# Kernel optimization log

Measured on AMD Instinct MI355X. Metric: run time of the kernel, lower is better.

## Reference

```python
import jax, jax.numpy as jnp
import numpy as np

B, C_IN, L = 8, 12, 4096
D = 64        # mamba_in_ch
DI = 2 * D    # d_inner (expand=2)
DS = 16       # d_state
DC = 4        # d_conv
DTR = 4       # dt_rank = ceil(D/16)
R = 10        # pixel-shuffle / upsample factor
K = 15        # big conv kernel size

def _p(key, shape, scale=0.05):
    return (jax.random.normal(key, shape) * scale).astype(jnp.float32)

def setup_inputs() -> dict:
    key = jax.random.key(0)
    ks = jax.random.split(key, 12)
    return dict(
        x=jax.random.normal(ks[0], (B, C_IN, L), jnp.float32),
        conv_in_w=_p(ks[1], (D, C_IN, K)), conv_in_b=jnp.zeros((D,), jnp.float32),
        in_proj_w=_p(ks[2], (2 * DI, D)),
        dw_conv_w=_p(ks[3], (DI, 1, DC)), dw_conv_b=jnp.zeros((DI,), jnp.float32),
        x_proj_w=_p(ks[4], (DTR + 2 * DS, DI)),
        dt_proj_w=_p(ks[5], (DI, DTR)), dt_proj_b=_p(ks[6], (DI,)),
        A_log=jnp.log(jnp.tile(jnp.arange(1, DS + 1, dtype=jnp.float32)[None, :], (DI, 1))),
        D_ssm=jnp.ones((DI,), jnp.float32),
        out_proj_w=_p(ks[7], (D, DI)),
        conv_merge_w=_p(ks[8], (D, D, K)), conv_merge_b=jnp.zeros((D,), jnp.float32),
        bn_gamma=jnp.ones((D,), jnp.float32), bn_beta=jnp.zeros((D,), jnp.float32),
        conv_ps1_w=_p(ks[9], (R * C_IN, D, K)), conv_ps1_b=jnp.zeros((R * C_IN,), jnp.float32),
    )

def conv1d(x, w, b, pad_l, pad_r, groups=1):
    out = jax.lax.conv_general_dilated(x, w, (1,), [(pad_l, pad_r)],
        dimension_numbers=('NCH', 'OIH', 'NCH'), feature_group_count=groups)
    return out + b[None, :, None]

def mamba_layer(x, in_proj_w, dw_w, dw_b, x_proj_w, dt_proj_w, dt_proj_b, A_log, D_ssm, out_proj_w):
    # x: (B, L, D)
    xz = jnp.einsum('bld,ed->ble', x, in_proj_w)          # (B,L,2*DI)
    xs, z = jnp.split(xz, 2, axis=-1)
    xc = jnp.transpose(xs, (0, 2, 1))                      # (B,DI,L)
    xc = conv1d(xc, dw_w, dw_b, DC - 1, 0, groups=DI)      # causal depthwise conv, truncated to L
    xs = jax.nn.silu(jnp.transpose(xc, (0, 2, 1)))         # (B,L,DI)
    dbl = jnp.einsum('bld,ed->ble', xs, x_proj_w)          # (B,L,DTR+2*DS)
    dt, Bm, Cm = jnp.split(dbl, [DTR, DTR + DS], axis=-1)
    dt = jax.nn.softplus(jnp.einsum('blr,dr->bld', dt, dt_proj_w) + dt_proj_b)  # (B,L,DI)
    A = -jnp.exp(A_log)                                    # (DI,DS)
    dA = jnp.exp(dt[..., None] * A)                        # (B,L,DI,DS)
    dBx = dt[..., None] * Bm[:, :, None, :] * xs[..., None]

    def step(h, inputs):
        dA_t, dBx_t, C_t = inputs                          # (B,DI,DS),(B,DI,DS),(B,DS)
        h = dA_t * h + dBx_t
        y = jnp.einsum('bds,bs->bd', h, C_t)
        return h, y

    h0 = jnp.zeros((x.shape[0], DI, DS), x.dtype)
    _, ys = jax.lax.scan(step, h0,
        (jnp.transpose(dA, (1, 0, 2, 3)), jnp.transpose(dBx, (1, 0, 2, 3)), jnp.transpose(Cm, (1, 0, 2))))
    y = jnp.transpose(ys, (1, 0, 2)) + xs * D_ssm          # (B,L,DI)
    y = y * jax.nn.silu(z)
    return jnp.einsum('bld,ed->ble', y, out_proj_w)        # (B,L,D)

def reference(x, conv_in_w, conv_in_b, in_proj_w, dw_conv_w, dw_conv_b, x_proj_w,
              dt_proj_w, dt_proj_b, A_log, D_ssm, out_proj_w,
              conv_merge_w, conv_merge_b, bn_gamma, bn_beta, conv_ps1_w, conv_ps1_b):
    pad = (K - 1) // 2
    x_in = jax.nn.leaky_relu(conv1d(x, conv_in_w, conv_in_b, pad, pad), 0.01)  # (B,64,L)
    xm = jnp.transpose(x_in, (0, 2, 1))
    xm = xm + mamba_layer(xm, in_proj_w, dw_conv_w, dw_conv_b, x_proj_w,
                          dt_proj_w, dt_proj_b, A_log, D_ssm, out_proj_w)     # n_layer=1, residual
    xm = jnp.transpose(xm, (0, 2, 1))                                          # (B,64,L)
    xmerge = conv1d(xm, conv_merge_w, conv_merge_b, pad, pad)
    mean = jnp.mean(xmerge, axis=(0, 2), keepdims=True)                        # BatchNorm1d (training stats)
    var = jnp.var(xmerge, axis=(0, 2), keepdims=True)
    xmerge = (xmerge - mean) * jax.lax.rsqrt(var + 1e-5) * bn_gamma[None, :, None] + bn_beta[None, :, None]
    xmerge = xmerge + x_in
    xp = conv1d(xmerge, conv_ps1_w, conv_ps1_b, pad, pad)                      # (B,120,L)
    # PixelShuffle1D(r=10): (B, r*Cout, L) -> (B, Cout, L*r)
    Bn, ch, Ln = xp.shape
    ps = xp.reshape(Bn, R, ch // R, Ln).transpose(0, 2, 3, 1).reshape(Bn, ch // R, Ln * R)
    # F.interpolate(x, scale_factor=10, mode='linear', align_corners=False)
    out_len = L * R
    src = jnp.maximum((jnp.arange(out_len, dtype=jnp.float32) + 0.5) / R - 0.5, 0.0)
    i0 = jnp.minimum(jnp.floor(src).astype(jnp.int32), L - 1)
    i1 = jnp.minimum(i0 + 1, L - 1)
    frac = src - i0.astype(jnp.float32)
    up = x[..., i0] * (1.0 - frac) + x[..., i1] * frac
    return ps + up
```

## Files before the change

kernel.cpp:

```cpp
#include <hip/hip_runtime.h>
#include <math.h>

#define BB 8
#define CIN 12
#define LL 4096
#define DD 64
#define DIx 128
#define DSx 16
#define RR 10
#define KK 15
#define NCH 256
#define CLEN 16
#define OUTL 40960

typedef __attribute__((ext_vector_type(8))) short s8v;
typedef __attribute__((ext_vector_type(8))) __bf16 b8v;
typedef __attribute__((ext_vector_type(4))) float f4v;
union frag_u { s8v s; b8v b; };

__device__ __forceinline__ unsigned short f2b(float f) {
    unsigned int u = __float_as_uint(f);
    u = (u + 0x7fffu + ((u >> 16) & 1u)) >> 16;
    return (unsigned short)u;
}
__device__ __forceinline__ float b2f(unsigned short h) {
    return __uint_as_float(((unsigned int)h) << 16);
}

template<int CI, int CO, int COT, bool LEAKY>
__global__ __launch_bounds__(256) void k_conv(const float* __restrict__ in,
        const float* __restrict__ w, const float* __restrict__ bias,
        float* __restrict__ out) {
    const int LT = 1024;
    int tid = threadIdx.x;
    int bid = blockIdx.x;
    const int nlt = LL / LT;
    const int ncog = CO / COT;
    int lt = bid % nlt;
    int cog = (bid / nlt) % ncog;
    int b = bid / (nlt * ncog);
    int l0 = lt * LT + tid * 4;
    int co0 = cog * COT;

    float acc[COT][4];
#pragma unroll
    for (int c = 0; c < COT; ++c) {
        float bv = bias[co0 + c];
#pragma unroll
        for (int j = 0; j < 4; ++j) acc[c][j] = bv;
    }
    for (int ci = 0; ci < CI; ++ci) {
        const float* inp = in + ((size_t)b * CI + ci) * LL;
        float in20[20];
#pragma unroll
        for (int q = 0; q < 5; ++q) {
            int gi = l0 - 8 + q * 4;
            if (gi >= 0 && gi + 3 < LL) {
                float4 v = *(const float4*)(inp + gi);
                in20[q*4+0] = v.x; in20[q*4+1] = v.y;
                in20[q*4+2] = v.z; in20[q*4+3] = v.w;
            } else {
#pragma unroll
                for (int j = 0; j < 4; ++j) {
                    int g = gi + j;
                    in20[q*4+j] = (g >= 0 && g < LL) ? inp[g] : 0.f;
                }
            }
        }
#pragma unroll
        for (int c = 0; c < COT; ++c) {
            const float* wp = w + ((size_t)(co0 + c) * CI + ci) * KK;
#pragma unroll
            for (int k = 0; k < KK; ++k) {
                float wv = wp[k];
#pragma unroll
                for (int j = 0; j < 4; ++j)
                    acc[c][j] += wv * in20[j + k + 1];
            }
        }
    }
#pragma unroll
    for (int c = 0; c < COT; ++c) {
        float r[4];
#pragma unroll
        for (int j = 0; j < 4; ++j) {
            float v = acc[c][j];
            if (LEAKY) v = (v >= 0.f) ? v : 0.01f * v;
            r[j] = v;
        }
        *(float4*)(out + ((size_t)b * CO + co0 + c) * LL + l0) =
            make_float4(r[0], r[1], r[2], r[3]);
    }
}

template<int CO_REAL, int NCOB>
__global__ __launch_bounds__(256) void k_wprep(const float* __restrict__ w,
        unsigned short* __restrict__ wp) {
    int idx = blockIdx.x * 256 + threadIdx.x;
    if (idx >= 15 * NCOB * 1024) return;
    int j = idx & 7;
    int lane = (idx >> 3) & 63;
    int cis = (idx >> 9) & 1;
    int rest = idx >> 10;
    int cob = rest % NCOB;
    int kk = rest / NCOB;
    int co = cob * 16 + (lane & 15);
    int ci = cis * 32 + ((lane >> 4) << 3) + j;
    float val = (co < CO_REAL) ? w[((size_t)co * 64 + ci) * KK + kk] : 0.f;
    wp[idx] = f2b(val);
}

template<int CO_REAL, int NCOB, int MODE>
__global__ __launch_bounds__(256) void k_convmfma(
        const unsigned short* __restrict__ xt,
        const unsigned short* __restrict__ wp,
        const float* __restrict__ bias, void* __restrict__ outv) {
    __shared__ unsigned short in_lds[142 * 72];
    const int NCOT = NCOB / 4;
    int tid = threadIdx.x;
    int bid = blockIdx.x;
    int lt = bid & 31;
    int cot = (bid >> 5) % NCOT;
    int b = bid / (32 * NCOT);
    int l0 = lt * 128;
#pragma unroll
    for (int i = 0; i < 5; ++i) {
        int q = i * 256 + tid;
        if (q < 1136) {
            int r = q >> 3, c8 = (q & 7) * 8;
            int gl = l0 - 7 + r;
            s8v v = {0,0,0,0,0,0,0,0};
            if (gl >= 0 && gl < LL)
                v = *(const s8v*)&xt[((size_t)b * LL + gl) * 64 + c8];
            *(s8v*)&in_lds[r * 72 + c8] = v;
        }
    }
    __syncthreads();
    int lane = tid & 63, wv = tid >> 6;
    int corow = (lane >> 4) << 2;
    f4v acc[4][2];
#pragma unroll
    for (int mt = 0; mt < 4; ++mt) {
#pragma unroll
        for (int r = 0; r < 4; ++r) {
            int co = cot * 64 + mt * 16 + corow + r;
            float bv = (co < CO_REAL) ? bias[co] : 0.f;
            acc[mt][0][r] = bv;
            acc[mt][1][r] = bv;
        }
    }
    int bcol = lane & 15;
    int cig = (lane >> 4) << 3;
    for (int k = 0; k < KK; ++k) {
#pragma unroll
        for (int cis = 0; cis < 2; ++cis) {
            frag_u a[4], bf[2];
#pragma unroll
            for (int mt = 0; mt < 4; ++mt)
                a[mt].s = *(const s8v*)&wp[((((k * NCOB + cot * 4 + mt) * 2 + cis) << 9)
                                           + (lane << 3))];
#pragma unroll
            for (int nt = 0; nt < 2; ++nt)
                bf[nt].s = *(const s8v*)&in_lds[(wv * 32 + nt * 16 + bcol + k) * 72
                                               + cis * 32 + cig];
#pragma unroll
            for (int mt = 0; mt < 4; ++mt)
#pragma unroll
                for (int nt = 0; nt < 2; ++nt)
                    acc[mt][nt] = __builtin_amdgcn_mfma_f32_16x16x32_bf16(
                        a[mt].b, bf[nt].b, acc[mt][nt], 0, 0, 0);
        }
    }
#pragma unroll
    for (int mt = 0; mt < 4; ++mt)
#pragma unroll
        for (int nt = 0; nt < 2; ++nt) {
            int l = l0 + wv * 32 + nt * 16 + bcol;
#pragma unroll
            for (int r = 0; r < 4; ++r) {
                int co = cot * 64 + mt * 16 + corow + r;
                if (co < CO_REAL) {
                    if (MODE == 0)
                        ((float*)outv)[((size_t)b * CO_REAL + co) * LL + l] = acc[mt][nt][r];
                    else
                        ((unsigned short*)outv)[((size_t)b * CO_REAL + co) * LL + l]
                            = f2b(acc[mt][nt][r]);
                }
            }
        }
}

__global__ __launch_bounds__(256) void k_bnpart(const float* __restrict__ xm,
        float* __restrict__ stats) {
    int c = blockIdx.x >> 3, b = blockIdx.x & 7;
    const float* p = xm + ((size_t)b * DD + c) * LL;
    int tid = threadIdx.x;
    float s = 0.f, ss = 0.f;
#pragma unroll
    for (int it = 0; it < 4; ++it) {
        float4 v = *(const float4*)(p + (size_t)(it * 256 + tid) * 4);
        s  += v.x + v.y + v.z + v.w;
        ss += v.x*v.x + v.y*v.y + v.z*v.z + v.w*v.w;
    }
    for (int o = 32; o > 0; o >>= 1) {
        s  += __shfl_down(s, o);
        ss += __shfl_down(ss, o);
    }
    __shared__ float red[8];
    int wid = tid >> 6;
    if ((tid & 63) == 0) { red[wid] = s; red[4 + wid] = ss; }
    __syncthreads();
    if (tid == 0) {
        atomicAdd(&stats[c], red[0] + red[1] + red[2] + red[3]);
        atomicAdd(&stats[64 + c], red[4] + red[5] + red[6] + red[7]);
    }
}

__global__ __launch_bounds__(256) void k_gemm_inproj(const float* __restrict__ A,
        const float* __restrict__ W, unsigned short* __restrict__ C) {
    __shared__ float At[64 * 132];
    __shared__ float Wt[64 * 132];
    int tid = threadIdx.x;
    int bid = blockIdx.x;
    int nb = bid & 1;
    int mb = bid >> 1;
    int row0 = mb * 128;
    int n0 = nb * 128;
    int b = row0 >> 12;
    int l0 = row0 & 4095;
#pragma unroll
    for (int it = 0; it < 8; ++it) {
        int idx = it * 256 + tid;
        int k = idx >> 5, m4 = (idx & 31) * 4;
        float4 v = *(const float4*)(A + ((size_t)b * DD + k) * LL + l0 + m4);
        *(float4*)&At[k * 132 + m4] = v;
    }
#pragma unroll
    for (int it = 0; it < 8; ++it) {
        int lin = it * 1024 + tid * 4;
        int n = lin >> 6, k = lin & 63;
        float4 v = *(const float4*)(W + (size_t)(n0 + n) * 64 + k);
        Wt[(k+0)*132 + n] = v.x; Wt[(k+1)*132 + n] = v.y;
        Wt[(k+2)*132 + n] = v.z; Wt[(k+3)*132 + n] = v.w;
    }
    __syncthreads();
    int tx = tid & 15, ty = tid >> 4;
    float acc[2][2][4][4] = {};
#pragma unroll 4
    for (int k = 0; k < 64; ++k) {
        float4 aLo = *(float4*)&At[k*132 + ty*4];
        float4 aHi = *(float4*)&At[k*132 + 64 + ty*4];
        float4 bLo = *(float4*)&Wt[k*132 + tx*4];
        float4 bHi = *(float4*)&Wt[k*132 + 64 + tx*4];
        float a0[4] = {aLo.x, aLo.y, aLo.z, aLo.w};
        float a1[4] = {aHi.x, aHi.y, aHi.z, aHi.w};
        float b0[4] = {bLo.x, bLo.y, bLo.z, bLo.w};
        float b1[4] = {bHi.x, bHi.y, bHi.z, bHi.w};
#pragma unroll
        for (int mm = 0; mm < 4; ++mm)
#pragma unroll
            for (int nn = 0; nn < 4; ++nn) {
                acc[0][0][mm][nn] += a0[mm] * b0[nn];
                acc[0][1][mm][nn] += a0[mm] * b1[nn];
                acc[1][0][mm][nn] += a1[mm] * b0[nn];
                acc[1][1][mm][nn] += a1[mm] * b1[nn];
            }
    }
#pragma unroll
    for (int qm = 0; qm < 2; ++qm)
#pragma unroll
        for (int mm = 0; mm < 4; ++mm) {
            int row = row0 + qm*64 + ty*4 + mm;
#pragma unroll
            for (int qn = 0; qn < 2; ++qn) {
                unsigned short o[4];
#pragma unroll
                for (int nn = 0; nn < 4; ++nn) o[nn] = f2b(acc[qm][qn][mm][nn]);
                *(uint2*)&C[(size_t)row * 256 + n0 + qn*64 + tx*4] = *(uint2*)o;
            }
        }
}

template<int NW>
__global__ __launch_bounds__(256) void k_gemm64dw(
        const unsigned short* __restrict__ xzb,
        const float* __restrict__ dww, const float* __restrict__ dwb,
        const float* __restrict__ W, float* __restrict__ out) {
    __shared__ float At[64 * 132];
    __shared__ float Wt[64 * 68];
    __shared__ float sdw[128][4];
    __shared__ float sbias[128];
    int tid = threadIdx.x;
    int row0 = blockIdx.x * 128;
    int l0 = row0 & 4095;
    if (tid < 128) {
        *(float4*)&sdw[tid][0] = *(const float4*)(dww + tid * 4);
        sbias[tid] = dwb[tid];
    }
    int tx = tid & 15, ty = tid >> 4;
    float acc[2][4][4] = {};
#pragma unroll
    for (int kt = 0; kt < 2; ++kt) {
        __syncthreads();
#pragma unroll
        for (int it = 0; it < 4; ++it) {
            int task = it * 256 + tid;
            int m = task >> 3;
            int k8 = (task & 7) * 8;
            int d0 = kt * 64 + k8;
            float s[8];
#pragma unroll
            for (int j = 0; j < 8; ++j) s[j] = sbias[d0 + j];
#pragma unroll
            for (int tap = 0; tap < 4; ++tap) {
                if (l0 + m - 3 + tap >= 0) {
                    s8v xv = *(const s8v*)&xzb[(size_t)(row0 + m - 3 + tap) * 256 + d0];
#pragma unroll
                    for (int j = 0; j < 8; ++j)
                        s[j] += b2f((unsigned short)xv[j]) * sdw[d0 + j][tap];
                }
            }
#pragma unroll
            for (int j = 0; j < 8; ++j) {
                float v = s[j];
                At[(k8 + j) * 132 + m] = v / (1.f + __expf(-v));
            }
        }
#pragma unroll
        for (int it = 0; it < 4; ++it) {
            int lin = it * 1024 + tid * 4;
            int n = lin >> 6, k = lin & 63;
            float4 v = make_float4(0.f, 0.f, 0.f, 0.f);
            if (n < NW)
                v = *(const float4*)(W + (size_t)n * 128 + kt*64 + k);
            Wt[(k+0)*68 + n] = v.x; Wt[(k+1)*68 + n] = v.y;
            Wt[(k+2)*68 + n] = v.z; Wt[(k+3)*68 + n] = v.w;
        }
        __syncthreads();
#pragma unroll 4
        for (int k = 0; k < 64; ++k) {
            float4 aLo = *(float4*)&At[k*132 + ty*4];
            float4 aHi = *(float4*)&At[k*132 + 64 + ty*4];
            float4 b4  = *(float4*)&Wt[k*68 + tx*4];
            float a0[4] = {aLo.x, aLo.y, aLo.z, aLo.w};
            float a1[4] = {aHi.x, aHi.y, aHi.z, aHi.w};
            float bv[4] = {b4.x, b4.y, b4.z, b4.w};
#pragma unroll
            for (int mm = 0; mm < 4; ++mm)
#pragma unroll
                for (int nn = 0; nn < 4; ++nn) {
                    acc[0][mm][nn] += a0[mm] * bv[nn];
                    acc[1][mm][nn] += a1[mm] * bv[nn];
                }
        }
    }
#pragma unroll
    for (int qm = 0; qm < 2; ++qm)
#pragma unroll
        for (int mm = 0; mm < 4; ++mm) {
            int row = row0 + qm*64 + ty*4 + mm;
            *(float4*)(out + (size_t)row * 64 + tx*4) =
                make_float4(acc[qm][mm][0], acc[qm][mm][1],
                            acc[qm][mm][2], acc[qm][mm][3]);
        }
}

__global__ __launch_bounds__(256) void k_gemm64_tr(
        const unsigned short* __restrict__ A, const float* __restrict__ W,
        const float* __restrict__ res, unsigned short* __restrict__ out) {
    __shared__ float smem[13312];
    float* At = smem;
    float* Wt = smem + 64*132;
    int tid = threadIdx.x;
    int row0 = blockIdx.x * 128;
    int tx = tid & 15, ty = tid >> 4;
    int b = row0 >> 12, l0 = row0 & 4095;
    float acc[2][4][4] = {};
#pragma unroll
    for (int kt = 0; kt < 2; ++kt) {
        __syncthreads();
#pragma unroll
        for (int it = 0; it < 4; ++it) {
            int task = it * 256 + tid;
            int m = task >> 3;
            int k8 = (task & 7) * 8;
            s8v v = *(const s8v*)&A[(size_t)(row0 + m) * 128 + kt*64 + k8];
#pragma unroll
            for (int j = 0; j < 8; ++j)
                At[(k8 + j) * 132 + m] = b2f((unsigned short)v[j]);
        }
#pragma unroll
        for (int it = 0; it < 4; ++it) {
            int lin = it * 1024 + tid * 4;
            int n = lin >> 6, k = lin & 63;
            float4 v = *(const float4*)(W + (size_t)n * 128 + kt*64 + k);
            Wt[(k+0)*68 + n] = v.x; Wt[(k+1)*68 + n] = v.y;
            Wt[(k+2)*68 + n] = v.z; Wt[(k+3)*68 + n] = v.w;
        }
        __syncthreads();
#pragma unroll 4
        for (int k = 0; k < 64; ++k) {
            float4 aLo = *(float4*)&At[k*132 + ty*4];
            float4 aHi = *(float4*)&At[k*132 + 64 + ty*4];
            float4 b4  = *(float4*)&Wt[k*68 + tx*4];
            float a0[4] = {aLo.x, aLo.y, aLo.z, aLo.w};
            float a1[4] = {aHi.x, aHi.y, aHi.z, aHi.w};
            float bv[4] = {b4.x, b4.y, b4.z, b4.w};
#pragma unroll
            for (int mm = 0; mm < 4; ++mm)
#pragma unroll
                for (int nn = 0; nn < 4; ++nn) {
                    acc[0][mm][nn] += a0[mm] * bv[nn];
                    acc[1][mm][nn] += a1[mm] * bv[nn];
                }
        }
    }
    __syncthreads();
    float* tile = smem;
    unsigned short* resb = (unsigned short*)(smem + 8704);
#pragma unroll
    for (int qm = 0; qm < 2; ++qm)
#pragma unroll
        for (int mm = 0; mm < 4; ++mm) {
            int lrow = qm*64 + ty*4 + mm;
            *(float4*)&tile[lrow*68 + tx*4] = make_float4(
                acc[qm][mm][0], acc[qm][mm][1], acc[qm][mm][2], acc[qm][mm][3]);
        }
#pragma unroll
    for (int it = 0; it < 8; ++it) {
        int idx = it * 256 + tid;
        int d = idx >> 5, l4 = (idx & 31) * 4;
        float4 rv = *(const float4*)(res + ((size_t)b * DD + d) * LL + l0 + l4);
        resb[(l4+0)*72 + d] = f2b(rv.x);
        resb[(l4+1)*72 + d] = f2b(rv.y);
        resb[(l4+2)*72 + d] = f2b(rv.z);
        resb[(l4+3)*72 + d] = f2b(rv.w);
    }
    __syncthreads();
#pragma unroll
    for (int it = 0; it < 4; ++it) {
        int idx = it * 256 + tid;
        int l = idx >> 3, c8 = (idx & 7) * 8;
        unsigned short o[8];
#pragma unroll
        for (int j = 0; j < 8; ++j)
            o[j] = f2b(tile[l*68 + c8 + j] + b2f(resb[l*72 + c8 + j]));
        *(s8v*)&out[((size_t)b * LL + l0 + l) * 64 + c8] = *(s8v*)o;
    }
}

__global__ __launch_bounds__(256) void k_scan1(
        const unsigned short* __restrict__ xzb, const float* __restrict__ dbl,
        const float* __restrict__ dww, const float* __restrict__ dwb,
        const float* __restrict__ dtw, const float* __restrict__ dtbias,
        const float* __restrict__ A_log, float* __restrict__ P,
        float* __restrict__ Q) {
    __shared__ float sdbl[2][CLEN][64];
    int tid = threadIdx.x;
    int bid = blockIdx.x;
    int b = bid >> 7;
    int cpair = bid & 127;
    int half = tid >> 7;
    int d = tid & 127;
    int c = cpair * 2 + half;
    {
        const float4* src = (const float4*)(dbl +
            ((size_t)b * LL + (size_t)cpair * 2 * CLEN) * 64);
        float4* dst = (float4*)&sdbl[0][0][0];
#pragma unroll
        for (int i = 0; i < 2; ++i) dst[i * 256 + tid] = src[i * 256 + tid];
    }
    __syncthreads();
    float4 w4 = *(const float4*)(dtw + d * 4);
    float dbias = dtbias[d];
    float4 cw = *(const float4*)(dww + d * 4);
    float cbias = dwb[d];
    const float LOG2E = 1.4426950408889634f;
    float Ads2[16], h[16], p[16];
#pragma unroll
    for (int s = 0; s < 16; ++s) {
        Ads2[s] = -__expf(A_log[d * DSx + s]) * LOG2E;
        h[s] = 0.f; p[s] = 1.f;
    }
    int l0 = c * CLEN;
    const unsigned short* px = xzb + ((size_t)b * LL + l0) * 256 + d;
    float w0 = 0.f, w1 = 0.f, w2 = 0.f;
    if (l0) { w0 = b2f(px[-768]); w1 = b2f(px[-512]); w2 = b2f(px[-256]); }
    for (int t = 0; t < CLEN; ++t) {
        float cur = b2f(px[(size_t)t * 256]);
        float sv = cbias + w0*cw.x + w1*cw.y + w2*cw.z + cur*cw.w;
        float xs = sv / (1.f + __expf(-sv));
        w0 = w1; w1 = w2; w2 = cur;
        float4 di = *(const float4*)&sdbl[half][t][0];
        float dtv = di.x*w4.x + di.y*w4.y + di.z*w4.z + di.w*w4.w + dbias;
        dtv = (dtv > 15.f) ? dtv : __logf(1.f + __expf(dtv));
        float dx = dtv * xs;
#pragma unroll
        for (int s = 0; s < 16; ++s) {
            float da = __builtin_amdgcn_exp2f(dtv * Ads2[s]);
            h[s] = da * h[s] + dx * sdbl[half][t][4 + s];
            p[s] *= da;
        }
    }
    float* Pp = P + (size_t)c * 16384 + (size_t)(b * 128 + d) * 16;
    float* Qp = Q + (size_t)c * 16384 + (size_t)(b * 128 + d) * 16;
#pragma unroll
    for (int s4 = 0; s4 < 4; ++s4) {
        *(float4*)(Pp + s4*4) = make_float4(p[s4*4], p[s4*4+1], p[s4*4+2], p[s4*4+3]);
        *(float4*)(Qp + s4*4) = make_float4(h[s4*4], h[s4*4+1], h[s4*4+2], h[s4*4+3]);
    }
}

__global__ __launch_bounds__(256) void k_scan2(const float* __restrict__ P,
        const float* __restrict__ Q, float* __restrict__ Hin,
        float* __restrict__ stats) {
    int chain = blockIdx.x * 256 + threadIdx.x;
    if (blockIdx.x == 0 && threadIdx.x < 128) stats[threadIdx.x] = 0.f;
    float carry = 0.f;
    for (int c = 0; c < NCH; ++c) {
        Hin[(size_t)c * 16384 + chain] = carry;
        carry = P[(size_t)c * 16384 + chain] * carry + Q[(size_t)c * 16384 + chain];
    }
}

__global__ __launch_bounds__(256) void k_scan3(
        const unsigned short* __restrict__ xzb, const float* __restrict__ dbl,
        const float* __restrict__ dww, const float* __restrict__ dwb,
        const float* __restrict__ dtw, const float* __restrict__ dtbias,
        const float* __restrict__ A_log, const float* __restrict__ Hin,
        const float* __restrict__ Dssm, unsigned short* __restrict__ ymb) {
    __shared__ float sdbl[2][CLEN][64];
    int tid = threadIdx.x;
    int bid = blockIdx.x;
    int b = bid >> 7;
    int cpair = bid & 127;
    int half = tid >> 7;
    int d = tid & 127;
    int c = cpair * 2 + half;
    {
        const float4* src = (const float4*)(dbl +
            ((size_t)b * LL + (size_t)cpair * 2 * CLEN) * 64);
        float4* dst = (float4*)&sdbl[0][0][0];
#pragma unroll
        for (int i = 0; i < 2; ++i) dst[i * 256 + tid] = src[i * 256 + tid];
    }
    __syncthreads();
    float4 w4 = *(const float4*)(dtw + d * 4);
    float dbias = dtbias[d];
    float4 cw = *(const float4*)(dww + d * 4);
    float cbias = dwb[d];
    float Dv = Dssm[d];
    const float LOG2E = 1.4426950408889634f;
    float Ads2[16], h[16];
#pragma unroll
    for (int s = 0; s < 16; ++s)
        Ads2[s] = -__expf(A_log[d * DSx + s]) * LOG2E;
    const float* Hp = Hin + (size_t)c * 16384 + (size_t)(b * 128 + d) * 16;
#pragma unroll
    for (int s4 = 0; s4 < 4; ++s4) {
        float4 hv = *(const float4*)(Hp + s4*4);
        h[s4*4+0] = hv.x; h[s4*4+1] = hv.y; h[s4*4+2] = hv.z; h[s4*4+3] = hv.w;
    }
    int l0 = c * CLEN;
    size_t rowbase = (size_t)b * LL + l0;
    const unsigned short* px = xzb + rowbase * 256 + d;
    const unsigned short* pz = xzb + rowbase * 256 + 128 + d;
    unsigned short* pym = ymb + rowbase * 128 + d;
    float w0 = 0.f, w1 = 0.f, w2 = 0.f;
    if (l0) { w0 = b2f(px[-768]); w1 = b2f(px[-512]); w2 = b2f(px[-256]); }
    for (int t = 0; t < CLEN; ++t) {
        float cur = b2f(px[(size_t)t * 256]);
        float sv = cbias + w0*cw.x + w1*cw.y + w2*cw.z + cur*cw.w;
        float xs = sv / (1.f + __expf(-sv));
        w0 = w1; w1 = w2; w2 = cur;
        float4 di = *(const float4*)&sdbl[half][t][0];
        float dtv = di.x*w4.x + di.y*w4.y + di.z*w4.z + di.w*w4.w + dbias;
        dtv = (dtv > 15.f) ? dtv : __logf(1.f + __expf(dtv));
        float dx = dtv * xs;
        float y0 = 0.f, y1 = 0.f;
#pragma unroll
        for (int s = 0; s < 8; ++s) {
            float da = __builtin_amdgcn_exp2f(dtv * Ads2[s]);
            h[s] = da * h[s] + dx * sdbl[half][t][4 + s];
            y0 += h[s] * sdbl[half][t][20 + s];
        }
#pragma unroll
        for (int s = 8; s < 16; ++s) {
            float da = __builtin_amdgcn_exp2f(dtv * Ads2[s]);
            h[s] = da * h[s] + dx * sdbl[half][t][4 + s];
            y1 += h[s] * sdbl[half][t][20 + s];
        }
        float y = y0 + y1 + xs * Dv;
        float zv = b2f(pz[(size_t)t * 256]);
        y *= zv / (1.f + __expf(-zv));
        pym[(size_t)t * 128] = f2b(y);
    }
}

__global__ __launch_bounds__(256) void k_bnapply_t(const float* __restrict__ xm,
        const float* __restrict__ stats, const float* __restrict__ gamma,
        const float* __restrict__ beta, const float* __restrict__ xin,
        unsigned short* __restrict__ xf) {
    __shared__ float t[64][65];
    int tid = threadIdx.x;
    int b = blockIdx.x >> 6;
    int l0 = (blockIdx.x & 63) * 64;
    const float inv = 1.f / (float)(BB * LL);
#pragma unroll
    for (int it = 0; it < 16; ++it) {
        int idx = it * 256 + tid;
        int c = idx >> 6, l = idx & 63;
        float mean = stats[c] * inv;
        float var  = stats[64 + c] * inv - mean * mean;
        float g = gamma[c] * rsqrtf(var + 1e-5f);
        float sh = beta[c] - mean * g;
        size_t addr = ((size_t)b * DD + c) * LL + l0 + l;
        t[c][l] = xm[addr] * g + sh + xin[addr];
    }
    __syncthreads();
#pragma unroll
    for (int it = 0; it < 2; ++it) {
        int idx = it * 256 + tid;
        int l = idx >> 3, c8 = (idx & 7) * 8;
        unsigned short o[8];
#pragma unroll
        for (int j = 0; j < 8; ++j) o[j] = f2b(t[c8 + j][l]);
        *(s8v*)&xf[((size_t)b * LL + l0 + l) * 64 + c8] = *(s8v*)o;
    }
}

__global__ __launch_bounds__(256) void k_final(const unsigned short* __restrict__ xp,
        const float* __restrict__ x, float* __restrict__ out) {
    __shared__ float xps[10][257];
    __shared__ float xr[258];
    int tid = threadIdx.x;
    int bid = blockIdx.x;
    int lt = bid & 15;
    int c = (bid >> 4) % 12;
    int b = bid / (16 * 12);
    int l0 = lt * 256;
#pragma unroll
    for (int r = 0; r < 10; ++r)
        xps[r][tid] = b2f(xp[((size_t)b * 120 + r * 12 + c) * LL + l0 + tid]);
    const float* xrow = x + ((size_t)b * 12 + c) * LL;
    for (int i = tid; i < 258; i += 256) {
        int g = l0 - 1 + i;
        g = (g < 0) ? 0 : ((g > LL - 1) ? LL - 1 : g);
        xr[i] = xrow[g];
    }
    __syncthreads();
    size_t obase = ((size_t)b * 12 + c) * OUTL + (size_t)l0 * 10;
#pragma unroll
    for (int u = 0; u < 10; ++u) {
        int j = u * 256 + tid;
        int jg = l0 * 10 + j;
        int l = j / 10, r = j - l * 10;
        float ps = xps[r][l];
        float src = ((float)jg + 0.5f) * 0.1f - 0.5f;
        src = fmaxf(src, 0.f);
        int i0 = (int)src;
        if (i0 > LL - 1) i0 = LL - 1;
        int i1 = (i0 + 1 < LL) ? i0 + 1 : LL - 1;
        float frac = src - (float)i0;
        float up = xr[i0 - l0 + 1] * (1.f - frac) + xr[i1 - l0 + 1] * frac;
        out[obase + j] = ps + up;
    }
}

extern "C" void kernel_launch(void* const* d_in, const int* in_sizes, int n_in,
                              void* d_out, int out_size, void* d_ws, size_t ws_size,
                              hipStream_t stream) {
    const float* x          = (const float*)d_in[0];
    const float* conv_in_w  = (const float*)d_in[1];
    const float* conv_in_b  = (const float*)d_in[2];
    const float* in_proj_w  = (const float*)d_in[3];
    const float* dw_w       = (const float*)d_in[4];
    const float* dw_b       = (const float*)d_in[5];
    const float* x_proj_w   = (const float*)d_in[6];
    const float* dt_w       = (const float*)d_in[7];
    const float* dt_b       = (const float*)d_in[8];
    const float* A_log      = (const float*)d_in[9];
    const float* Dssm       = (const float*)d_in[10];
    const float* out_proj_w = (const float*)d_in[11];
    const float* cm_w       = (const float*)d_in[12];
    const float* cm_b       = (const float*)d_in[13];
    const float* bn_g       = (const float*)d_in[14];
    const float* bn_be      = (const float*)d_in[15];
    const float* ps_w       = (const float*)d_in[16];
    const float* ps_b       = (const float*)d_in[17];

    float* ws = (float*)d_ws;
    float* xin_bdl = ws;
    unsigned short* xzb = (unsigned short*)(ws + 2097152);
    float* dbl64   = ws + 6291456;
    float* P       = ws + 8388608;
    float* Q       = ws + 12582912;
    float* Hin     = ws + 16777216;
    float* stats   = ws + 20971520;
    unsigned short* ymb = (unsigned short*)(ws + 20971648);
    unsigned short* xmt = (unsigned short*)(ws + 23068800);
    float* xmerge  = ws + 24117376;
    unsigned short* xf  = (unsigned short*)(ws + 26214528);
    unsigned short* wp_ps = (unsigned short*)(ws + 27263104);
    unsigned short* wp_mg = (unsigned short*)(ws + 27324544);
    unsigned short* xpb = (unsigned short*)(ws + 27355264);

    k_conv<CIN, 64, 2, true><<<1024, 256, 0, stream>>>(x, conv_in_w, conv_in_b, xin_bdl);
    k_gemm_inproj<<<512, 256, 0, stream>>>(xin_bdl, in_proj_w, xzb);
    k_gemm64dw<36><<<256, 256, 0, stream>>>(xzb, dw_w, dw_b, x_proj_w, dbl64);
    k_scan1<<<1024, 256, 0, stream>>>(xzb, dbl64, dw_w, dw_b, dt_w, dt_b, A_log, P, Q);
    k_scan2<<<64, 256, 0, stream>>>(P, Q, Hin, stats);
    k_scan3<<<1024, 256, 0, stream>>>(xzb, dbl64, dw_w, dw_b, dt_w, dt_b, A_log, Hin,
                                      Dssm, ymb);
    k_wprep<120, 8><<<480, 256, 0, stream>>>(ps_w, wp_ps);
    k_wprep<64, 4><<<240, 256, 0, stream>>>(cm_w, wp_mg);
    k_gemm64_tr<<<256, 256, 0, stream>>>(ymb, out_proj_w, xin_bdl, xmt);
    k_convmfma<64, 4, 0><<<256, 256, 0, stream>>>(xmt, wp_mg, cm_b, xmerge);
    k_bnpart<<<512, 256, 0, stream>>>(xmerge, stats);
    k_bnapply_t<<<512, 256, 0, stream>>>(xmerge, stats, bn_g, bn_be, xin_bdl, xf);
    k_convmfma<120, 8, 1><<<512, 256, 0, stream>>>(xf, wp_ps, ps_b, xpb);
    k_final<<<1536, 256, 0, stream>>>(xpb, x, (float*)d_out);
}
```

Before: 304.4 us.

## Fuse pixel-shuffle conv with shuffle/upsample epilogue and merge weight-prep kernels

Replaces the separate bf16 pixel-shuffle conv output plus the final shuffle/interpolate kernel with a single kernel. It computes all 120 output channels for a 64-sample tile, stages the results in LDS, and writes the shuffled, upsampled sum directly to the output with float4 stores. The aim is to avoid the global round trip of the intermediate tensor and one launch. The two weight-prep launches are also merged into one. In exchange, each block now does more MFMA work per tile, with a different wave mapping and 8 accumulators, which may change occupancy.

After: 311.2 us. 1.02x slower.

```diff
diff --git a/kernel.cpp b/kernel.cpp
--- a/kernel.cpp
+++ b/kernel.cpp
@@ -93,11 +93,17 @@
     }
 }
 
-template<int CO_REAL, int NCOB>
-__global__ __launch_bounds__(256) void k_wprep(const float* __restrict__ w,
-        unsigned short* __restrict__ wp) {
+__global__ __launch_bounds__(256) void k_wprep_all(const float* __restrict__ wps,
+        const float* __restrict__ wmg, unsigned short* __restrict__ wp_ps,
+        unsigned short* __restrict__ wp_mg) {
     int idx = blockIdx.x * 256 + threadIdx.x;
-    if (idx >= 15 * NCOB * 1024) return;
+    const float* w; unsigned short* wp; int NCOB, CO_REAL;
+    if (idx < 122880) { w = wps; wp = wp_ps; NCOB = 8; CO_REAL = 120; }
+    else {
+        idx -= 122880;
+        if (idx >= 61440) return;
+        w = wmg; wp = wp_mg; NCOB = 4; CO_REAL = 64;
+    }
     int j = idx & 7;
     int lane = (idx >> 3) & 63;
     int cis = (idx >> 9) & 1;
@@ -110,11 +116,11 @@
     wp[idx] = f2b(val);
 }
 
-template<int CO_REAL, int NCOB, int MODE>
+template<int CO_REAL, int NCOB>
 __global__ __launch_bounds__(256) void k_convmfma(
         const unsigned short* __restrict__ xt,
         const unsigned short* __restrict__ wp,
-        const float* __restrict__ bias, void* __restrict__ outv) {
+        const float* __restrict__ bias, float* __restrict__ out) {
     __shared__ unsigned short in_lds[142 * 72];
     const int NCOT = NCOB / 4;
     int tid = threadIdx.x;
@@ -179,15 +185,106 @@
 #pragma unroll
             for (int r = 0; r < 4; ++r) {
                 int co = cot * 64 + mt * 16 + corow + r;
-                if (co < CO_REAL) {
-                    if (MODE == 0)
-                        ((float*)outv)[((size_t)b * CO_REAL + co) * LL + l] = acc[mt][nt][r];
-                    else
-                        ((unsigned short*)outv)[((size_t)b * CO_REAL + co) * LL + l]
-                            = f2b(acc[mt][nt][r]);
-                }
-            }
-        }
+                if (co < CO_REAL)
+                    out[((size_t)b * CO_REAL + co) * LL + l] = acc[mt][nt][r];
+            }
+        }
+}
+
+__global__ __launch_bounds__(256) void k_convps(
+        const unsigned short* __restrict__ xt,
+        const unsigned short* __restrict__ wp,
+        const float* __restrict__ bias, const float* __restrict__ x,
+        float* __restrict__ out) {
+    __shared__ char smem[19552];
+    unsigned short* in_lds = (unsigned short*)smem;
+    int tid = threadIdx.x;
+    int bid = blockIdx.x;
+    int lt = bid & 63;
+    int b = bid >> 6;
+    int l0 = lt * 64;
+#pragma unroll
+    for (int i = 0; i < 3; ++i) {
+        int q = i * 256 + tid;
+        if (q < 624) {
+            int r = q >> 3, c8 = (q & 7) * 8;
+            int gl = l0 - 7 + r;
+            s8v v = {0,0,0,0,0,0,0,0};
+            if (gl >= 0 && gl < LL)
+                v = *(const s8v*)&xt[((size_t)b * LL + gl) * 64 + c8];
+            *(s8v*)&in_lds[r * 72 + c8] = v;
+        }
+    }
+    __syncthreads();
+    int lane = tid & 63, wv = tid >> 6;
+    int corow = (lane >> 4) << 2;
+    int bcol = lane & 15;
+    int cig = (lane >> 4) << 3;
+    f4v acc[8];
+#pragma unroll
+    for (int mt = 0; mt < 8; ++mt)
+#pragma unroll
+        for (int r = 0; r < 4; ++r) {
+            int co = mt * 16 + corow + r;
+            acc[mt][r] = (co < 120) ? bias[co] : 0.f;
+        }
+    for (int k = 0; k < KK; ++k) {
+#pragma unroll
+        for (int cis = 0; cis < 2; ++cis) {
+            frag_u bf;
+            bf.s = *(const s8v*)&in_lds[(wv * 16 + bcol + k) * 72 + cis * 32 + cig];
+#pragma unroll
+            for (int mt = 0; mt < 8; ++mt) {
+                frag_u a;
+                a.s = *(const s8v*)&wp[(((k * 8 + mt) * 2 + cis) << 9) + (lane << 3)];
+                acc[mt] = __builtin_amdgcn_mfma_f32_16x16x32_bf16(
+                    a.b, bf.b, acc[mt], 0, 0, 0);
+            }
+        }
+    }
+    __syncthreads();
+    unsigned short* tile = (unsigned short*)smem;
+    float* xr = (float*)(smem + 16384);
+    {
+        int l = wv * 16 + bcol;
+#pragma unroll
+        for (int mt = 0; mt < 8; ++mt)
+#pragma unroll
+            for (int r = 0; r < 4; ++r)
+                tile[l * 128 + mt * 16 + corow + r] = f2b(acc[mt][r]);
+    }
+    for (int q = tid; q < 792; q += 256) {
+        int c = q / 66, i = q - c * 66;
+        int g = l0 - 1 + i;
+        g = (g < 0) ? 0 : ((g > LL - 1) ? LL - 1 : g);
+        xr[c * 66 + i] = x[((size_t)b * 12 + c) * LL + g];
+    }
+    __syncthreads();
+    size_t obase = (size_t)b * 12 * OUTL + (size_t)l0 * 10;
+#pragma unroll
+    for (int q8 = 0; q8 < 8; ++q8) {
+        int idx = q8 * 256 + tid;
+        if (idx < 1920) {
+            int c = idx / 160;
+            int j = (idx - c * 160) * 4;
+            float o4[4];
+#pragma unroll
+            for (int u = 0; u < 4; ++u) {
+                int jj = j + u;
+                int l = jj / 10, r = jj - l * 10;
+                float ps = b2f(tile[l * 128 + r * 12 + c]);
+                float src = ((float)(l0 * 10 + jj) + 0.5f) * 0.1f - 0.5f;
+                src = fmaxf(src, 0.f);
+                int i0 = (int)src;
+                if (i0 > LL - 1) i0 = LL - 1;
+                int i1 = (i0 + 1 < LL) ? i0 + 1 : LL - 1;
+                float frac = src - (float)i0;
+                o4[u] = ps + xr[c * 66 + (i0 - l0 + 1)] * (1.f - frac)
+                           + xr[c * 66 + (i1 - l0 + 1)] * frac;
+            }
+            *(float4*)&out[obase + (size_t)c * OUTL + j] = *(float4*)o4;
+        }
+    }
 }
 
 __global__ __launch_bounds__(256) void k_bnpart(const float* __restrict__ xm,
@@ -626,44 +723,6 @@
 #pragma unroll
         for (int j = 0; j < 8; ++j) o[j] = f2b(t[c8 + j][l]);
         *(s8v*)&xf[((size_t)b * LL + l0 + l) * 64 + c8] = *(s8v*)o;
-    }
-}
-
-__global__ __launch_bounds__(256) void k_final(const unsigned short* __restrict__ xp,
-        const float* __restrict__ x, float* __restrict__ out) {
-    __shared__ float xps[10][257];
-    __shared__ float xr[258];
-    int tid = threadIdx.x;
-    int bid = blockIdx.x;
-    int lt = bid & 15;
-    int c = (bid >> 4) % 12;
-    int b = bid / (16 * 12);
-    int l0 = lt * 256;
-#pragma unroll
-    for (int r = 0; r < 10; ++r)
-        xps[r][tid] = b2f(xp[((size_t)b * 120 + r * 12 + c) * LL + l0 + tid]);
-    const float* xrow = x + ((size_t)b * 12 + c) * LL;
-    for (int i = tid; i < 258; i += 256) {
-        int g = l0 - 1 + i;
-        g = (g < 0) ? 0 : ((g > LL - 1) ? LL - 1 : g);
-        xr[i] = xrow[g];
-    }
-    __syncthreads();
-    size_t obase = ((size_t)b * 12 + c) * OUTL + (size_t)l0 * 10;
-#pragma unroll
-    for (int u = 0; u < 10; ++u) {
-        int j = u * 256 + tid;
-        int jg = l0 * 10 + j;
-        int l = j / 10, r = j - l * 10;
-        float ps = xps[r][l];
-        float src = ((float)jg + 0.5f) * 0.1f - 0.5f;
-        src = fmaxf(src, 0.f);
-        int i0 = (int)src;
-        if (i0 > LL - 1) i0 = LL - 1;
-        int i1 = (i0 + 1 < LL) ? i0 + 1 : LL - 1;
-        float frac = src - (float)i0;
-        float up = xr[i0 - l0 + 1] * (1.f - frac) + xr[i1 - l0 + 1] * frac;
-        out[obase + j] = ps + up;
     }
 }
 
@@ -703,7 +762,6 @@
     unsigned short* xf  = (unsigned short*)(ws + 26214528);
     unsigned short* wp_ps = (unsigned short*)(ws + 27263104);
     unsigned short* wp_mg = (unsigned short*)(ws + 27324544);
-    unsigned short* xpb = (unsigned short*)(ws + 27355264);
 
     k_conv<CIN, 64, 2, true><<<1024, 256, 0, stream>>>(x, conv_in_w, conv_in_b, xin_bdl);
     k_gemm_inproj<<<512, 256, 0, stream>>>(xin_bdl, in_proj_w, xzb);
@@ -712,12 +770,10 @@
     k_scan2<<<64, 256, 0, stream>>>(P, Q, Hin, stats);
     k_scan3<<<1024, 256, 0, stream>>>(xzb, dbl64, dw_w, dw_b, dt_w, dt_b, A_log, Hin,
                                       Dssm, ymb);
-    k_wprep<120, 8><<<480, 256, 0, stream>>>(ps_w, wp_ps);
-    k_wprep<64, 4><<<240, 256, 0, stream>>>(cm_w, wp_mg);
+    k_wprep_all<<<720, 256, 0, stream>>>(ps_w, cm_w, wp_ps, wp_mg);
     k_gemm64_tr<<<256, 256, 0, stream>>>(ymb, out_proj_w, xin_bdl, xmt);
-    k_convmfma<64, 4, 0><<<256, 256, 0, stream>>>(xmt, wp_mg, cm_b, xmerge);
+    k_convmfma<64, 4><<<256, 256, 0, stream>>>(xmt, wp_mg, cm_b, xmerge);
     k_bnpart<<<512, 256, 0, stream>>>(xmerge, stats);
     k_bnapply_t<<<512, 256, 0, stream>>>(xmerge, stats, bn_g, bn_be, xin_bdl, xf);
-    k_convmfma<120, 8, 1><<<512, 256, 0, stream>>>(xf, wp_ps, ps_b, xpb);
-    k_final<<<1536, 256, 0, stream>>>(xpb, x, (float*)d_out);
-}
+    k_convps<<<512, 256, 0, stream>>>(xf, wp_ps, ps_b, x, (float*)d_out);
+}
```
